# Kernel optimization log

Measured on AMD Instinct MI355X. Metric: run time of the kernel, lower is better.

Reference implementation:

```python
import jax, jax.numpy as jnp
import numpy as np

N_NODES = 50000
N_EDGES = 800000
NEG_SLOPE = 0.2  # PyG GATConv default negative_slope


def setup_inputs() -> dict:
    key = jax.random.key(0)
    ks = jax.random.split(key, 10)
    d_in, hid, heads = 128, 32, 8

    def glorot(k, shape):
        fan_in, fan_out = shape[0], shape[-1]
        s = jnp.sqrt(2.0 / (fan_in + fan_out)).astype(jnp.float32)
        return jax.random.normal(k, shape, jnp.float32) * s

    return {
        "x": jax.random.normal(ks[0], (N_NODES, d_in), jnp.float32),
        "edge_index": jax.random.randint(ks[1], (2, N_EDGES), 0, N_NODES),
        "W1": glorot(ks[2], (d_in, heads * hid)),
        "a1_src": glorot(ks[3], (heads, hid)),
        "a1_dst": glorot(ks[4], (heads, hid)),
        "b1": jnp.zeros((heads * hid,), jnp.float32),
        "W2": glorot(ks[5], (heads * hid, hid)),
        "a2_src": glorot(ks[6], (1, hid)),
        "a2_dst": glorot(ks[7], (1, hid)),
        "b2": jnp.zeros((hid,), jnp.float32),
    }


def _gat_layer(x, src, dst, W, a_src, a_dst, b, concat):
    # PyG GATConv: h = x @ W, split into heads; alpha_e = softmax_over_dst(
    #   leaky_relu(<h[src], a_src> + <h[dst], a_dst>)); out = scatter-sum alpha*h[src].
    N = x.shape[0]
    H, D = a_src.shape
    h = (x @ W).reshape(N, H, D)                      # [N, H, D]
    score_s = jnp.einsum("nhd,hd->nh", h, a_src)      # [N, H]
    score_d = jnp.einsum("nhd,hd->nh", h, a_dst)
    e = jax.nn.leaky_relu(score_s[src] + score_d[dst], NEG_SLOPE)  # [E, H]
    # numerically-stable softmax over incoming edges per destination node
    m = jax.ops.segment_max(e, dst, num_segments=N)
    ex = jnp.exp(e - m[dst])
    denom = jax.ops.segment_sum(ex, dst, num_segments=N)
    alpha = ex / (denom[dst] + 1e-16)                 # [E, H]
    out = jax.ops.segment_sum(alpha[:, :, None] * h[src], dst, num_segments=N)  # [N, H, D]
    out = out.reshape(N, H * D) if concat else out[:, 0]
    return out + b


def reference(x, edge_index, W1, a1_src, a1_dst, b1, W2, a2_src, a2_dst, b2):
    N = x.shape[0]
    # PyG GATConv add_self_loops=True
    loop = jnp.arange(N, dtype=edge_index.dtype)
    src = jnp.concatenate([edge_index[0], loop])
    dst = jnp.concatenate([edge_index[1], loop])
    h = _gat_layer(x, src, dst, W1, a1_src, a1_dst, b1, concat=True)
    h = jax.nn.relu(h)
    # dropout(p=0.4) is identity in eval mode (deterministic reference)
    return _gat_layer(h, src, dst, W2, a2_src, a2_dst, b2, concat=False)
```

## Files before the change

kernel.cpp:

```cpp
#include <hip/hip_runtime.h>
#include <hip/hip_fp16.h>
#include <math.h>

#define N_NODES 50000
#define N_EDGES 800000
#define E_TOT (N_EDGES + N_NODES)
#define N_RT 3125
#define CAP 64

typedef unsigned int uint;
typedef unsigned short ushort;
typedef float f32x4 __attribute__((ext_vector_type(4)));
typedef short v8s __attribute__((ext_vector_type(8)));

__device__ __forceinline__ ushort f2bf(float f) {
    uint u = __float_as_uint(f);
    return (ushort)((u + 0x7FFFu + ((u >> 16) & 1u)) >> 16);
}
__device__ __forceinline__ float bf2f(ushort u) {
    return __uint_as_float((uint)u << 16);
}
__device__ __forceinline__ float bflo(uint v) { return __uint_as_float(v << 16); }
__device__ __forceinline__ float bfhi(uint v) { return __uint_as_float(v & 0xFFFF0000u); }

__device__ __forceinline__ int kmap(int g, int j) {
    return ((j >> 2) << 4) + (g << 2) + (j & 3);
}


__global__ void wprep_k(const float* __restrict__ W1, const float* __restrict__ a1s,
                        const float* __restrict__ a1d, const float* __restrict__ W2,
                        ushort* __restrict__ W1f, ushort* __restrict__ W2b,
                        ushort* __restrict__ W2r, ushort* __restrict__ Abf,
                        ushort* __restrict__ Arf, int* __restrict__ cnt) {
    for (int i = blockIdx.x * 256 + threadIdx.x; i < N_NODES; i += 21 * 256)
        cnt[i] = 0;

    if (blockIdx.x < 16) {
        int idx = blockIdx.x * 256 + threadIdx.x;
        int lane = idx & 63, ks = (idx >> 6) & 3, ct = idx >> 8;
        int g = lane >> 4, col = ct * 16 + (lane & 15);
        ushort us[8];
        #pragma unroll
        for (int j = 0; j < 8; j++) {
            int k = ks * 32 + kmap(g, j);
            us[j] = f2bf(W1[(size_t)k * 256 + col]);
        }
        uint4 pk;
        pk.x = (uint)us[0] | ((uint)us[1] << 16);
        pk.y = (uint)us[2] | ((uint)us[3] << 16);
        pk.z = (uint)us[4] | ((uint)us[5] << 16);
        pk.w = (uint)us[6] | ((uint)us[7] << 16);
        *((uint4*)(W1f + ((size_t)(ct * 4 + ks) * 64 + lane) * 8)) = pk;
    } else if (blockIdx.x < 20) {
        int idx = (blockIdx.x - 16) * 256 + threadIdx.x;
        int lane = idx & 63, ks = (idx >> 6) & 7, ct = idx >> 9;
        int g = lane >> 4, col = ct * 16 + (lane & 15);
        ushort ub[8], ur[8];
        #pragma unroll
        for (int j = 0; j < 8; j++) {
            int k = ks * 32 + kmap(g, j);
            float v = W2[(size_t)k * 32 + col];
            ub[j] = f2bf(v);
            ur[j] = f2bf(v - bf2f(ub[j]));
        }
        uint4 pb, pr;
        pb.x = (uint)ub[0] | ((uint)ub[1] << 16);
        pb.y = (uint)ub[2] | ((uint)ub[3] << 16);
        pb.z = (uint)ub[4] | ((uint)ub[5] << 16);
        pb.w = (uint)ub[6] | ((uint)ub[7] << 16);
        pr.x = (uint)ur[0] | ((uint)ur[1] << 16);
        pr.y = (uint)ur[2] | ((uint)ur[3] << 16);
        pr.z = (uint)ur[4] | ((uint)ur[5] << 16);
        pr.w = (uint)ur[6] | ((uint)ur[7] << 16);
        *((uint4*)(W2b + ((size_t)(ct * 8 + ks) * 64 + lane) * 8)) = pb;
        *((uint4*)(W2r + ((size_t)(ct * 8 + ks) * 64 + lane) * 8)) = pr;
    } else if (blockIdx.x == 20) {
        int t = threadIdx.x;
        int lane = t & 63, ks = t >> 6;
        int jcol = lane & 15, g = lane >> 4;
        int hh = (jcol < 8) ? jcol : jcol - 8;
        const float* a = (jcol < 8) ? (a1s + hh * 32) : (a1d + hh * 32);
        ushort ub[8], ur[8];
        #pragma unroll
        for (int j = 0; j < 8; j++) {
            int k = ks * 32 + kmap(g, j);
            const float* wrow = W1 + (size_t)k * 256 + hh * 32;
            float v = 0.f;
            #pragma unroll 8
            for (int d = 0; d < 32; d++) v = fmaf(wrow[d], a[d], v);
            ub[j] = f2bf(v);
            ur[j] = f2bf(v - bf2f(ub[j]));
        }
        uint4 pb, pr;
        pb.x = (uint)ub[0] | ((uint)ub[1] << 16);
        pb.y = (uint)ub[2] | ((uint)ub[3] << 16);
        pb.z = (uint)ub[4] | ((uint)ub[5] << 16);
        pb.w = (uint)ub[6] | ((uint)ub[7] << 16);
        pr.x = (uint)ur[0] | ((uint)ur[1] << 16);
        pr.y = (uint)ur[2] | ((uint)ur[3] << 16);
        pr.z = (uint)ur[4] | ((uint)ur[5] << 16);
        pr.w = (uint)ur[6] | ((uint)ur[7] << 16);
        *((uint4*)(Abf + ((size_t)ks * 64 + lane) * 8)) = pb;
        *((uint4*)(Arf + ((size_t)ks * 64 + lane) * 8)) = pr;
    }
}


__global__ __launch_bounds__(256) void scat_k(const int* __restrict__ ei,
                                              int* __restrict__ cnt,
                                              ushort* __restrict__ csr) {
    int t = blockIdx.x * 256 + threadIdx.x;
    if (t < N_EDGES / 8) {
        int4 sv0 = ((const int4*)ei)[2 * t];
        int4 sv1 = ((const int4*)ei)[2 * t + 1];
        int4 dv0 = ((const int4*)(ei + N_EDGES))[2 * t];
        int4 dv1 = ((const int4*)(ei + N_EDGES))[2 * t + 1];
        int p0 = atomicAdd(&cnt[dv0.x], 1);
        int p1 = atomicAdd(&cnt[dv0.y], 1);
        int p2 = atomicAdd(&cnt[dv0.z], 1);
        int p3 = atomicAdd(&cnt[dv0.w], 1);
        int p4 = atomicAdd(&cnt[dv1.x], 1);
        int p5 = atomicAdd(&cnt[dv1.y], 1);
        int p6 = atomicAdd(&cnt[dv1.z], 1);
        int p7 = atomicAdd(&cnt[dv1.w], 1);
        if (p0 < CAP) csr[dv0.x * CAP + p0] = (ushort)sv0.x;
        if (p1 < CAP) csr[dv0.y * CAP + p1] = (ushort)sv0.y;
        if (p2 < CAP) csr[dv0.z * CAP + p2] = (ushort)sv0.z;
        if (p3 < CAP) csr[dv0.w * CAP + p3] = (ushort)sv0.w;
        if (p4 < CAP) csr[dv1.x * CAP + p4] = (ushort)sv1.x;
        if (p5 < CAP) csr[dv1.y * CAP + p5] = (ushort)sv1.y;
        if (p6 < CAP) csr[dv1.z * CAP + p6] = (ushort)sv1.z;
        if (p7 < CAP) csr[dv1.w * CAP + p7] = (ushort)sv1.w;
    } else if (t < N_EDGES / 8 + (N_NODES + 3) / 4) {
        int n0 = (t - N_EDGES / 8) * 4;
        int p[4];
        #pragma unroll
        for (int j = 0; j < 4; j++) {
            int n = n0 + j;
            p[j] = (n < N_NODES) ? atomicAdd(&cnt[n], 1) : CAP;
        }
        #pragma unroll
        for (int j = 0; j < 4; j++) {
            int n = n0 + j;
            if (n < N_NODES && p[j] < CAP) csr[n * CAP + p[j]] = (ushort)n;
        }
    }
}


__global__ __launch_bounds__(256) void fgemm1_k(
        const float* __restrict__ x, const ushort* __restrict__ W1f,
        const ushort* __restrict__ Abf, const ushort* __restrict__ Arf,
        ushort* __restrict__ h1u, float* __restrict__ s1s,
        float* __restrict__ s1d) {
    int lane = threadIdx.x & 63, wv = threadIdx.x >> 6;
    int rt = blockIdx.x * 4 + wv;
    if (rt >= N_RT) return;
    int r = lane & 15, g = lane >> 4;
    const float* xrow = x + ((size_t)rt * 16 + r) * 128;

    v8s xb[4], xr[4];
    #pragma unroll
    for (int ks = 0; ks < 4; ks++) {
        float4 fa = *((const float4*)(xrow + ks * 32 + g * 4));
        float4 fb = *((const float4*)(xrow + ks * 32 + 16 + g * 4));
        ushort b0 = f2bf(fa.x), b1 = f2bf(fa.y), b2 = f2bf(fa.z), b3 = f2bf(fa.w);
        ushort b4 = f2bf(fb.x), b5 = f2bf(fb.y), b6 = f2bf(fb.z), b7 = f2bf(fb.w);
        uint4 p;
        p.x = (uint)b0 | ((uint)b1 << 16);
        p.y = (uint)b2 | ((uint)b3 << 16);
        p.z = (uint)b4 | ((uint)b5 << 16);
        p.w = (uint)b6 | ((uint)b7 << 16);
        xb[ks] = *((v8s*)&p);
        ushort r0 = f2bf(fa.x - bf2f(b0)), r1 = f2bf(fa.y - bf2f(b1));
        ushort r2 = f2bf(fa.z - bf2f(b2)), r3 = f2bf(fa.w - bf2f(b3));
        ushort r4 = f2bf(fb.x - bf2f(b4)), r5 = f2bf(fb.y - bf2f(b5));
        ushort r6 = f2bf(fb.z - bf2f(b6)), r7 = f2bf(fb.w - bf2f(b7));
        uint4 q;
        q.x = (uint)r0 | ((uint)r1 << 16);
        q.y = (uint)r2 | ((uint)r3 << 16);
        q.z = (uint)r4 | ((uint)r5 << 16);
        q.w = (uint)r6 | ((uint)r7 << 16);
        xr[ks] = *((v8s*)&q);
    }

    f32x4 sacc = (f32x4){0.f, 0.f, 0.f, 0.f};
    const v8s* abp = (const v8s*)Abf;
    const v8s* arp = (const v8s*)Arf;
    #pragma unroll
    for (int ks = 0; ks < 4; ks++) {
        v8s ab = abp[ks * 64 + lane];
        v8s ar = arp[ks * 64 + lane];
        sacc = __builtin_amdgcn_mfma_f32_16x16x32_bf16(ab, xb[ks], sacc, 0, 0, 0);
        sacc = __builtin_amdgcn_mfma_f32_16x16x32_bf16(ar, xb[ks], sacc, 0, 0, 0);
        sacc = __builtin_amdgcn_mfma_f32_16x16x32_bf16(ab, xr[ks], sacc, 0, 0, 0);
    }
    {
        int row = rt * 16 + r;
        float4 sv;
        sv.x = sacc[0]; sv.y = sacc[1]; sv.z = sacc[2]; sv.w = sacc[3];
        if (g < 2) *((float4*)(s1s + (size_t)row * 8 + g * 4)) = sv;
        else       *((float4*)(s1d + (size_t)row * 8 + (g - 2) * 4)) = sv;
    }

    f32x4 acc[16];
    #pragma unroll
    for (int ct = 0; ct < 16; ct++) acc[ct] = (f32x4){0.f, 0.f, 0.f, 0.f};
    const v8s* bp = (const v8s*)W1f;
    #pragma unroll
    for (int ks = 0; ks < 4; ks++) {
        #pragma unroll
        for (int ct = 0; ct < 16; ct++) {
            v8s wf = bp[(ct * 4 + ks) * 64 + lane];
            acc[ct] = __builtin_amdgcn_mfma_f32_16x16x32_bf16(wf, xb[ks], acc[ct], 0, 0, 0);
        }
    }

    ushort* hrow = h1u + ((size_t)rt * 16 + r) * 256;
    #pragma unroll
    for (int ct = 0; ct < 16; ct++) {
        uint lo = (uint)f2bf(acc[ct][0]) | ((uint)f2bf(acc[ct][1]) << 16);
        uint hi = (uint)f2bf(acc[ct][2]) | ((uint)f2bf(acc[ct][3]) << 16);
        *((uint2*)(hrow + ct * 16 + g * 4)) = make_uint2(lo, hi);
    }
}


__global__ __launch_bounds__(256) void stats1_k(
        const ushort* __restrict__ csr, const int* __restrict__ cnt,
        const float* __restrict__ s1s, const float* __restrict__ s1d,
        __half* __restrict__ ebuf, float2* __restrict__ minv) {
    int n = blockIdx.x * 4 + (threadIdx.x >> 6);
    int lane = threadIdx.x & 63;
    int e8 = lane >> 3, h = lane & 7;
    int beg = n * CAP;
    int end = beg + min(cnt[n], CAP);
    float sd = s1d[n * 8 + h];
    float m = -3.4e38f, d = 0.f;
    for (int i = beg + e8; i < end; i += 8) {
        int s = csr[i];
        float e = s1s[s * 8 + h] + sd;
        e = (e >= 0.f) ? e : 0.2f * e;
        ebuf[(size_t)i * 8 + h] = __float2half(e);
        float mn = fmaxf(m, e);
        d = d * __expf(m - mn) + __expf(e - mn);
        m = mn;
    }
    #pragma unroll
    for (int mask = 8; mask <= 32; mask <<= 1) {
        float om = __shfl_xor(m, mask);
        float od = __shfl_xor(d, mask);
        float nm = fmaxf(m, om);
        d = d * __expf(m - nm) + od * __expf(om - nm);
        m = nm;
    }
    if (e8 == 0) {
        float2 o; o.x = m; o.y = 1.f / (d + 1e-16f);
        minv[n * 8 + h] = o;
    }
}


__global__ __launch_bounds__(256) void agg1_k(
        const ushort* __restrict__ csr, const int* __restrict__ cnt,
        const ushort* __restrict__ h1u, const __half* __restrict__ ebuf,
        const float2* __restrict__ minv, const float* __restrict__ b1,
        ushort* __restrict__ hrb) {
    int lane = threadIdx.x & 63;
    int n = blockIdx.x * 4 + (threadIdx.x >> 6);
    int h = lane >> 3;
    int beg = n * CAP;
    int end = beg + min(cnt[n], CAP);
    float2 mi = minv[n * 8 + h];
    float m = mi.x, inv = mi.y;
    const uint2* hv = (const uint2*)h1u;
    float acc0 = 0.f, acc1 = 0.f, acc2 = 0.f, acc3 = 0.f;
    int i = beg;
    for (; i + 3 < end; i += 4) {
        uint2 cs = *((const uint2*)(csr + i));
        int s0 = cs.x & 0xFFFF, s1 = cs.x >> 16;
        int s2 = cs.y & 0xFFFF, s3 = cs.y >> 16;
        float p0 = __expf(__half2float(ebuf[(size_t)i * 8 + h]) - m);
        float p1 = __expf(__half2float(ebuf[(size_t)(i + 1) * 8 + h]) - m);
        float p2 = __expf(__half2float(ebuf[(size_t)(i + 2) * 8 + h]) - m);
        float p3 = __expf(__half2float(ebuf[(size_t)(i + 3) * 8 + h]) - m);
        uint2 v0 = hv[(size_t)s0 * 64 + lane];
        uint2 v1 = hv[(size_t)s1 * 64 + lane];
        uint2 v2 = hv[(size_t)s2 * 64 + lane];
        uint2 v3 = hv[(size_t)s3 * 64 + lane];
        acc0 = fmaf(p0, bflo(v0.x), acc0);
        acc1 = fmaf(p0, bfhi(v0.x), acc1);
        acc2 = fmaf(p0, bflo(v0.y), acc2);
        acc3 = fmaf(p0, bfhi(v0.y), acc3);
        acc0 = fmaf(p1, bflo(v1.x), acc0);
        acc1 = fmaf(p1, bfhi(v1.x), acc1);
        acc2 = fmaf(p1, bflo(v1.y), acc2);
        acc3 = fmaf(p1, bfhi(v1.y), acc3);
        acc0 = fmaf(p2, bflo(v2.x), acc0);
        acc1 = fmaf(p2, bfhi(v2.x), acc1);
        acc2 = fmaf(p2, bflo(v2.y), acc2);
        acc3 = fmaf(p2, bfhi(v2.y), acc3);
        acc0 = fmaf(p3, bflo(v3.x), acc0);
        acc1 = fmaf(p3, bfhi(v3.x), acc1);
        acc2 = fmaf(p3, bflo(v3.y), acc2);
        acc3 = fmaf(p3, bfhi(v3.y), acc3);
    }
    for (; i < end; i++) {
        int s0 = csr[i];
        float p0 = __expf(__half2float(ebuf[(size_t)i * 8 + h]) - m);
        uint2 v0 = hv[(size_t)s0 * 64 + lane];
        acc0 = fmaf(p0, bflo(v0.x), acc0);
        acc1 = fmaf(p0, bfhi(v0.x), acc1);
        acc2 = fmaf(p0, bflo(v0.y), acc2);
        acc3 = fmaf(p0, bfhi(v0.y), acc3);
    }
    int c0 = 4 * lane;
    float4 bv = *((const float4*)(b1 + c0));
    float o0 = fmaxf(fmaf(acc0, inv, bv.x), 0.f);
    float o1 = fmaxf(fmaf(acc1, inv, bv.y), 0.f);
    float o2 = fmaxf(fmaf(acc2, inv, bv.z), 0.f);
    float o3 = fmaxf(fmaf(acc3, inv, bv.w), 0.f);
    uint lo = (uint)f2bf(o0) | ((uint)f2bf(o1) << 16);
    uint hi = (uint)f2bf(o2) | ((uint)f2bf(o3) << 16);
    ((uint2*)hrb)[(size_t)n * 64 + lane] = make_uint2(lo, hi);
}


__global__ __launch_bounds__(256) void gemm2m_k(
        const ushort* __restrict__ hrb, const ushort* __restrict__ W2b,
        const ushort* __restrict__ W2r, const float* __restrict__ a2s,
        const float* __restrict__ a2d, ushort* __restrict__ h2u,
        float* __restrict__ s2s, float* __restrict__ s2d) {
    int lane = threadIdx.x & 63, wv = threadIdx.x >> 6;
    int rt = blockIdx.x * 4 + wv;
    if (rt >= N_RT) return;
    int r = lane & 15, g = lane >> 4;
    int row = rt * 16 + r;
    const ushort* arow = hrb + (size_t)row * 256;

    v8s af[8];
    #pragma unroll
    for (int ks = 0; ks < 8; ks++) {
        uint2 u0 = *((const uint2*)(arow + ks * 32 + g * 4));
        uint2 u1 = *((const uint2*)(arow + ks * 32 + 16 + g * 4));
        uint4 p; p.x = u0.x; p.y = u0.y; p.z = u1.x; p.w = u1.y;
        af[ks] = *((v8s*)&p);
    }

    f32x4 acc[2];
    acc[0] = (f32x4){0.f, 0.f, 0.f, 0.f};
    acc[1] = (f32x4){0.f, 0.f, 0.f, 0.f};
    const v8s* wbp = (const v8s*)W2b;
    const v8s* wrp = (const v8s*)W2r;
    #pragma unroll
    for (int ks = 0; ks < 8; ks++) {
        #pragma unroll
        for (int ct = 0; ct < 2; ct++) {
            v8s wb = wbp[(ct * 8 + ks) * 64 + lane];
            v8s wr = wrp[(ct * 8 + ks) * 64 + lane];
            acc[ct] = __builtin_amdgcn_mfma_f32_16x16x32_bf16(wb, af[ks], acc[ct], 0, 0, 0);
            acc[ct] = __builtin_amdgcn_mfma_f32_16x16x32_bf16(wr, af[ks], acc[ct], 0, 0, 0);
        }
    }

    float ps = 0.f, pd = 0.f;
    #pragma unroll
    for (int ct = 0; ct < 2; ct++) {
        #pragma unroll
        for (int q = 0; q < 4; q++) {
            int c = ct * 16 + g * 4 + q;
            ps = fmaf(acc[ct][q], a2s[c], ps);
            pd = fmaf(acc[ct][q], a2d[c], pd);
        }
    }
    ps += __shfl_xor(ps, 16); ps += __shfl_xor(ps, 32);
    pd += __shfl_xor(pd, 16); pd += __shfl_xor(pd, 32);
    if (g == 0) { s2s[row] = ps; s2d[row] = pd; }

    #pragma unroll
    for (int ct = 0; ct < 2; ct++) {
        uint lo = (uint)f2bf(acc[ct][0]) | ((uint)f2bf(acc[ct][1]) << 16);
        uint hi = (uint)f2bf(acc[ct][2]) | ((uint)f2bf(acc[ct][3]) << 16);
        *((uint2*)(h2u + (size_t)row * 32 + ct * 16 + g * 4)) = make_uint2(lo, hi);
    }
}


__global__ __launch_bounds__(256) void agg2_k(
        const ushort* __restrict__ csr, const int* __restrict__ cnt,
        const ushort* __restrict__ h2u, const float* __restrict__ s2s,
        const float* __restrict__ s2d, const float* __restrict__ b2,
        float* __restrict__ out) {
    int lane = threadIdx.x & 63;
    int n = blockIdx.x * 4 + (threadIdx.x >> 6);
    int beg = n * CAP;
    int end = beg + min(cnt[n], CAP);
    float sd = s2d[n];

    float m = -3.4e38f, dd = 0.f;
    for (int i = beg + lane; i < end; i += 64) {
        float e = s2s[csr[i]] + sd;
        e = (e >= 0.f) ? e : 0.2f * e;
        float mn = fmaxf(m, e);
        dd = dd * __expf(m - mn) + __expf(e - mn);
        m = mn;
    }
    #pragma unroll
    for (int mask = 1; mask <= 32; mask <<= 1) {
        float om = __shfl_xor(m, mask);
        float od = __shfl_xor(dd, mask);
        float nm = fmaxf(m, om);
        dd = dd * __expf(m - nm) + od * __expf(om - nm);
        m = nm;
    }
    float inv = 1.f / (dd + 1e-16f);

    int e4 = lane >> 4, cp = lane & 15;
    float acc0 = 0.f, acc1 = 0.f;
    for (int c0 = beg; c0 < end; c0 += 64) {
        int i = c0 + lane;
        int sL = 0; float aL = 0.f;
        if (i < end) {
            sL = csr[i];
            float e = s2s[sL] + sd;
            e = (e >= 0.f) ? e : 0.2f * e;
            aL = __expf(e - m) * inv;
        }
        int nsub = min(64, end - c0);
        for (int el = 0; el < nsub; el += 4) {
            int local = el + e4;
            int se = __shfl(sL, local);
            float ae = __shfl(aL, local);
            uint v = *((const uint*)(h2u + (size_t)se * 32 + cp * 2));
            acc0 = fmaf(ae, bflo(v), acc0);
            acc1 = fmaf(ae, bfhi(v), acc1);
        }
    }
    acc0 += __shfl_xor(acc0, 16); acc0 += __shfl_xor(acc0, 32);
    acc1 += __shfl_xor(acc1, 16); acc1 += __shfl_xor(acc1, 32);
    if (lane < 16) {
        float2 bv = ((const float2*)b2)[cp];
        float2 o; o.x = acc0 + bv.x; o.y = acc1 + bv.y;
        ((float2*)(out + (size_t)n * 32))[cp] = o;
    }
}


extern "C" void kernel_launch(void* const* d_in, const int* in_sizes, int n_in,
                              void* d_out, int out_size, void* d_ws, size_t ws_size,
                              hipStream_t stream) {
    const float* x   = (const float*)d_in[0];
    const int*   ei  = (const int*)d_in[1];
    const float* W1  = (const float*)d_in[2];
    const float* a1s = (const float*)d_in[3];
    const float* a1d = (const float*)d_in[4];
    const float* b1  = (const float*)d_in[5];
    const float* W2  = (const float*)d_in[6];
    const float* a2s = (const float*)d_in[7];
    const float* a2d = (const float*)d_in[8];
    const float* b2  = (const float*)d_in[9];
    float* out = (float*)d_out;

    char* w = (char*)d_ws;
    ushort* h1u   = (ushort*)w; w += (size_t)N_NODES * 256 * 2;
    ushort* hrb   = (ushort*)w; w += (size_t)N_NODES * 256 * 2;
    ushort* W1f   = (ushort*)w; w += (size_t)16 * 4 * 64 * 8 * 2;
    ushort* Abf   = (ushort*)w; w += (size_t)4 * 64 * 8 * 2;
    ushort* Arf   = (ushort*)w; w += (size_t)4 * 64 * 8 * 2;
    ushort* W2b   = (ushort*)w; w += (size_t)2 * 8 * 64 * 8 * 2;
    ushort* W2r   = (ushort*)w; w += (size_t)2 * 8 * 64 * 8 * 2;
    ushort* h2u   = (ushort*)w; w += (size_t)N_NODES * 32 * 2;
    float* s1s    = (float*)w;  w += (size_t)N_NODES * 8 * 4;
    float* s1d    = (float*)w;  w += (size_t)N_NODES * 8 * 4;
    float* s2s    = (float*)w;  w += (size_t)N_NODES * 4;
    float* s2d    = (float*)w;  w += (size_t)N_NODES * 4;
    float2* minv  = (float2*)w; w += (size_t)N_NODES * 8 * 8;
    __half* ebuf  = (__half*)w; w += (size_t)N_NODES * CAP * 8 * 2;
    int* cnt    = (int*)w; w += (size_t)N_NODES * 4;
    ushort* csr = (ushort*)w; w += (size_t)N_NODES * CAP * 2;

    int nscat = (N_EDGES / 8 + (N_NODES + 3) / 4 + 255) / 256;

    wprep_k<<<21, 256, 0, stream>>>(W1, a1s, a1d, W2, W1f, W2b, W2r, Abf, Arf, cnt);
    scat_k<<<nscat, 256, 0, stream>>>(ei, cnt, csr);
    fgemm1_k<<<(N_RT + 3) / 4, 256, 0, stream>>>(x, W1f, Abf, Arf, h1u, s1s, s1d);
    stats1_k<<<N_NODES / 4, 256, 0, stream>>>(csr, cnt, s1s, s1d, ebuf, minv);
    agg1_k<<<N_NODES / 4, 256, 0, stream>>>(csr, cnt, h1u, ebuf, minv, b1, hrb);
    gemm2m_k<<<(N_RT + 3) / 4, 256, 0, stream>>>(hrb, W2b, W2r, a2s, a2d, h2u, s2s, s2d);
    agg2_k<<<N_NODES / 4, 256, 0, stream>>>(csr, cnt, h2u, s2s, s2d, b2, out);
}
```

Measured before the change: 223.5 us.

## Fuse softmax stats kernel into layer-1 aggregation using per-wave LDS scores

```diff
diff --git a/kernel.cpp b/kernel.cpp
--- a/kernel.cpp
+++ b/kernel.cpp
@@ -227,22 +227,27 @@
 }
 
 
-__global__ __launch_bounds__(256) void stats1_k(
+__global__ __launch_bounds__(256) void agg1_k(
         const ushort* __restrict__ csr, const int* __restrict__ cnt,
-        const float* __restrict__ s1s, const float* __restrict__ s1d,
-        __half* __restrict__ ebuf, float2* __restrict__ minv) {
-    int n = blockIdx.x * 4 + (threadIdx.x >> 6);
+        const ushort* __restrict__ h1u, const float* __restrict__ s1s,
+        const float* __restrict__ s1d, const float* __restrict__ b1,
+        ushort* __restrict__ hrb) {
+    __shared__ float els[4][CAP][8];
     int lane = threadIdx.x & 63;
-    int e8 = lane >> 3, h = lane & 7;
+    int wv = threadIdx.x >> 6;
+    int n = blockIdx.x * 4 + wv;
     int beg = n * CAP;
-    int end = beg + min(cnt[n], CAP);
-    float sd = s1d[n * 8 + h];
+    int deg = min(cnt[n], CAP);
+    int end = beg + deg;
+
+    int e8 = lane >> 3, h8 = lane & 7;
+    float sd = s1d[n * 8 + h8];
     float m = -3.4e38f, d = 0.f;
     for (int i = beg + e8; i < end; i += 8) {
         int s = csr[i];
-        float e = s1s[s * 8 + h] + sd;
+        float e = s1s[s * 8 + h8] + sd;
         e = (e >= 0.f) ? e : 0.2f * e;
-        ebuf[(size_t)i * 8 + h] = __float2half(e);
+        els[wv][i - beg][h8] = e;
         float mn = fmaxf(m, e);
         d = d * __expf(m - mn) + __expf(e - mn);
         m = mn;
@@ -255,36 +260,23 @@
         d = d * __expf(m - nm) + od * __expf(om - nm);
         m = nm;
     }
-    if (e8 == 0) {
-        float2 o; o.x = m; o.y = 1.f / (d + 1e-16f);
-        minv[n * 8 + h] = o;
-    }
-}
-
-
-__global__ __launch_bounds__(256) void agg1_k(
-        const ushort* __restrict__ csr, const int* __restrict__ cnt,
-        const ushort* __restrict__ h1u, const __half* __restrict__ ebuf,
-        const float2* __restrict__ minv, const float* __restrict__ b1,
-        ushort* __restrict__ hrb) {
-    int lane = threadIdx.x & 63;
-    int n = blockIdx.x * 4 + (threadIdx.x >> 6);
-    int h = lane >> 3;
-    int beg = n * CAP;
-    int end = beg + min(cnt[n], CAP);
-    float2 mi = minv[n * 8 + h];
-    float m = mi.x, inv = mi.y;
+    float inv = 1.f / (d + 1e-16f);
+    int hB = lane >> 3;
+    float mB = __shfl(m, hB);
+    float invB = __shfl(inv, hB);
+
     const uint2* hv = (const uint2*)h1u;
+    const float* ep = &els[wv][0][hB];
     float acc0 = 0.f, acc1 = 0.f, acc2 = 0.f, acc3 = 0.f;
-    int i = beg;
-    for (; i + 3 < end; i += 4) {
-        uint2 cs = *((const uint2*)(csr + i));
+    int j = 0;
+    for (; j + 3 < deg; j += 4) {
+        uint2 cs = *((const uint2*)(csr + beg + j));
         int s0 = cs.x & 0xFFFF, s1 = cs.x >> 16;
         int s2 = cs.y & 0xFFFF, s3 = cs.y >> 16;
-        float p0 = __expf(__half2float(ebuf[(size_t)i * 8 + h]) - m);
-        float p1 = __expf(__half2float(ebuf[(size_t)(i + 1) * 8 + h]) - m);
-        float p2 = __expf(__half2float(ebuf[(size_t)(i + 2) * 8 + h]) - m);
-        float p3 = __expf(__half2float(ebuf[(size_t)(i + 3) * 8 + h]) - m);
+        float p0 = __expf(ep[(j + 0) * 8] - mB);
+        float p1 = __expf(ep[(j + 1) * 8] - mB);
+        float p2 = __expf(ep[(j + 2) * 8] - mB);
+        float p3 = __expf(ep[(j + 3) * 8] - mB);
         uint2 v0 = hv[(size_t)s0 * 64 + lane];
         uint2 v1 = hv[(size_t)s1 * 64 + lane];
         uint2 v2 = hv[(size_t)s2 * 64 + lane];
@@ -306,9 +298,9 @@
         acc2 = fmaf(p3, bflo(v3.y), acc2);
         acc3 = fmaf(p3, bfhi(v3.y), acc3);
     }
-    for (; i < end; i++) {
-        int s0 = csr[i];
-        float p0 = __expf(__half2float(ebuf[(size_t)i * 8 + h]) - m);
+    for (; j < deg; j++) {
+        int s0 = csr[beg + j];
+        float p0 = __expf(ep[j * 8] - mB);
         uint2 v0 = hv[(size_t)s0 * 64 + lane];
         acc0 = fmaf(p0, bflo(v0.x), acc0);
         acc1 = fmaf(p0, bfhi(v0.x), acc1);
@@ -317,10 +309,10 @@
     }
     int c0 = 4 * lane;
     float4 bv = *((const float4*)(b1 + c0));
-    float o0 = fmaxf(fmaf(acc0, inv, bv.x), 0.f);
-    float o1 = fmaxf(fmaf(acc1, inv, bv.y), 0.f);
-    float o2 = fmaxf(fmaf(acc2, inv, bv.z), 0.f);
-    float o3 = fmaxf(fmaf(acc3, inv, bv.w), 0.f);
+    float o0 = fmaxf(fmaf(acc0, invB, bv.x), 0.f);
+    float o1 = fmaxf(fmaf(acc1, invB, bv.y), 0.f);
+    float o2 = fmaxf(fmaf(acc2, invB, bv.z), 0.f);
+    float o3 = fmaxf(fmaf(acc3, invB, bv.w), 0.f);
     uint lo = (uint)f2bf(o0) | ((uint)f2bf(o1) << 16);
     uint hi = (uint)f2bf(o2) | ((uint)f2bf(o3) << 16);
     ((uint2*)hrb)[(size_t)n * 64 + lane] = make_uint2(lo, hi);
@@ -475,8 +467,6 @@
     float* s1d    = (float*)w;  w += (size_t)N_NODES * 8 * 4;
     float* s2s    = (float*)w;  w += (size_t)N_NODES * 4;
     float* s2d    = (float*)w;  w += (size_t)N_NODES * 4;
-    float2* minv  = (float2*)w; w += (size_t)N_NODES * 8 * 8;
-    __half* ebuf  = (__half*)w; w += (size_t)N_NODES * CAP * 8 * 2;
     int* cnt    = (int*)w; w += (size_t)N_NODES * 4;
     ushort* csr = (ushort*)w; w += (size_t)N_NODES * CAP * 2;
 
@@ -485,8 +475,7 @@
     wprep_k<<<21, 256, 0, stream>>>(W1, a1s, a1d, W2, W1f, W2b, W2r, Abf, Arf, cnt);
     scat_k<<<nscat, 256, 0, stream>>>(ei, cnt, csr);
     fgemm1_k<<<(N_RT + 3) / 4, 256, 0, stream>>>(x, W1f, Abf, Arf, h1u, s1s, s1d);
-    stats1_k<<<N_NODES / 4, 256, 0, stream>>>(csr, cnt, s1s, s1d, ebuf, minv);
-    agg1_k<<<N_NODES / 4, 256, 0, stream>>>(csr, cnt, h1u, ebuf, minv, b1, hrb);
+    agg1_k<<<N_NODES / 4, 256, 0, stream>>>(csr, cnt, h1u, s1s, s1d, b1, hrb);
     gemm2m_k<<<(N_RT + 3) / 4, 256, 0, stream>>>(hrb, W2b, W2r, a2s, a2d, h2u, s2s, s2d);
     agg2_k<<<N_NODES / 4, 256, 0, stream>>>(csr, cnt, h2u, s2s, s2d, b2, out);
 }
```

Measured after the change: 212.8 us. 4.8% less time.
